# Performance work log

Hardware: AMD Instinct MI355X
Metric: run time of the kernel (lower is better)

The kernel has to match this reference:

```python
import jax, jax.numpy as jnp
import numpy as np

B, T, C = 8, 1024, 768
H = 12
HS = C // H  # 64


def setup_inputs() -> dict:
    key = jax.random.key(0)
    ks = jax.random.split(key, 6)
    s = C ** -0.5
    x = jax.random.normal(ks[0], (B, T, C), dtype=jnp.float32)
    Wq = jax.random.normal(ks[1], (H, C, HS), dtype=jnp.float32) * s
    Wk = jax.random.normal(ks[2], (H, C, HS), dtype=jnp.float32) * s
    Wv = jax.random.normal(ks[3], (H, C, HS), dtype=jnp.float32) * s
    Wproj = jax.random.normal(ks[4], (C, C), dtype=jnp.float32) * s
    bproj = jax.random.normal(ks[5], (C,), dtype=jnp.float32) * 0.01
    return {"x": x, "Wq": Wq, "Wk": Wk, "Wv": Wv, "Wproj": Wproj, "bproj": bproj}


def reference(x, Wq, Wk, Wv, Wproj, bproj):
    # per-head projections (equivalent to stacked per-head nn.Linear, bias=False)
    q = jnp.einsum('btc,hcd->bhtd', x, Wq)
    k = jnp.einsum('btc,hcd->bhtd', x, Wk)
    v = jnp.einsum('btc,hcd->bhtd', x, Wv)
    scale = HS ** -0.5
    scores = jnp.einsum('bhtd,bhsd->bhts', q, k) * scale  # [B,H,T,T]
    causal = jnp.tril(jnp.ones((T, T), dtype=bool))
    scores = jnp.where(causal, scores, -jnp.inf)
    weights = jax.nn.softmax(scores, axis=-1)
    out = jnp.einsum('bhts,bhsd->bhtd', weights, v)  # [B,H,T,HS]
    out = out.transpose(0, 2, 1, 3).reshape(B, T, C)  # concat heads
    # output projection (dropout is identity in eval mode)
    return out @ Wproj.T + bproj
```

## Files before the change

### kernel.cpp

```cpp
#include <hip/hip_runtime.h>
#include <hip/hip_bf16.h>


typedef short bf16x8 __attribute__((ext_vector_type(8)));
typedef short bf16x4 __attribute__((ext_vector_type(4)));
typedef float f32x4 __attribute__((ext_vector_type(4)));

static __device__ __forceinline__ unsigned short f2bf(float f) {
  unsigned int u = __float_as_uint(f);
  u += 0x7fffu + ((u >> 16) & 1u);
  return (unsigned short)(u >> 16);
}

static __device__ __forceinline__ unsigned int pk2bf(float a, float b) {
  union { __hip_bfloat162 h; unsigned int u; } c;
  c.h = __float22bfloat162_rn(make_float2(a, b));
  return c.u;
}

static __device__ __forceinline__ void gl_lds16(const void* g, void* l) {
  __builtin_amdgcn_global_load_lds(
      (const __attribute__((address_space(1))) unsigned int*)g,
      (__attribute__((address_space(3))) unsigned int*)l, 16, 0, 0);
}

__global__ __launch_bounds__(256) void k_prep(
    const float* __restrict__ x, const float* __restrict__ Wproj,
    const float* __restrict__ Wq, const float* __restrict__ Wk,
    const float* __restrict__ Wv,
    unsigned short* __restrict__ xb, unsigned short* __restrict__ wp,
    unsigned short* __restrict__ wt) {
  __shared__ float tb[64][65];
  const int bx = blockIdx.x;
  const int tid = threadIdx.x;
  if (bx < 6720) {
    const float* src = (bx < 6144) ? x : Wproj;
    unsigned short* dst = (bx < 6144) ? xb : wp;
    int i = (bx < 6144 ? bx : bx - 6144) * 256 + tid;
    float4 f = ((const float4*)src)[i];
    uint2 o;
    o.x = pk2bf(f.x, f.y);
    o.y = pk2bf(f.z, f.w);
    ((uint2*)dst)[i] = o;
    return;
  }
  const int idx = bx - 6720;
  const int c0 = (idx % 12) * 64;
  const int hq = idx / 12;
  const int qi = hq / 12, h = hq % 12;
  const float* W = (qi == 0) ? Wq : ((qi == 1) ? Wk : Wv);
  {
    int rowb = tid >> 4;
    int col4 = (tid & 15) * 4;
#pragma unroll
    for (int it = 0; it < 4; ++it) {
      int c = it * 16 + rowb;
      float4 f = *(const float4*)(W + (h * 768 + c0 + c) * 64 + col4);
      tb[c][col4] = f.x; tb[c][col4 + 1] = f.y; tb[c][col4 + 2] = f.z; tb[c][col4 + 3] = f.w;
    }
  }
  __syncthreads();
#pragma unroll
  for (int it = 0; it < 2; ++it) {
    int slot = it * 256 + tid;
    int d = slot >> 3, cg = (slot & 7) * 8;
    union { unsigned int u[4]; uint4 v; } o;
#pragma unroll
    for (int j = 0; j < 4; ++j)
      o.u[j] = pk2bf(tb[cg + 2 * j][d], tb[cg + 2 * j + 1][d]);
    *(uint4*)(wt + (qi * 768 + h * 64 + d) * 768 + c0 + cg) = o.v;
  }
}

__global__ __launch_bounds__(256) void k_gemm_qk(
    const unsigned short* __restrict__ xb,
    const unsigned short* __restrict__ wt,
    unsigned short* __restrict__ qkv) {
  __shared__ unsigned short As[128 * 32];
  __shared__ unsigned short Bs[128 * 32];
  const int tid = threadIdx.x;
  const int w = tid >> 6, lane = tid & 63, quad = lane >> 4, lr = lane & 15;
  const int wm = w >> 1, wn = w & 1;
  const int m0 = blockIdx.x * 128, n0 = blockIdx.y * 128;

  f32x4 acc[4][4] = {};

  const int srow = w * 16 + (lane >> 2);
  const int scol = (lane & 3) * 8;
  const unsigned short* ga0 = xb + (m0 + srow) * 768 + scol;
  const unsigned short* ga1 = ga0 + 64 * 768;
  const unsigned short* gb0 = wt + (n0 + srow) * 768 + scol;
  const unsigned short* gb1 = gb0 + 64 * 768;
  unsigned short* la0 = &As[(w * 16) * 32];
  unsigned short* la1 = la0 + 64 * 32;
  unsigned short* lb0 = &Bs[(w * 16) * 32];
  unsigned short* lb1 = lb0 + 64 * 32;

  for (int k0 = 0; k0 < 768; k0 += 32) {
    gl_lds16(ga0 + k0, la0);
    gl_lds16(ga1 + k0, la1);
    gl_lds16(gb0 + k0, lb0);
    gl_lds16(gb1 + k0, lb1);
    __syncthreads();
    bf16x8 af[4], bfr[4];
#pragma unroll
    for (int i = 0; i < 4; ++i)
      af[i] = *(const bf16x8*)(&As[(wm * 64 + i * 16 + lr) * 32 + quad * 8]);
#pragma unroll
    for (int j = 0; j < 4; ++j)
      bfr[j] = *(const bf16x8*)(&Bs[(wn * 64 + j * 16 + lr) * 32 + quad * 8]);
#pragma unroll
    for (int j = 0; j < 4; ++j)
#pragma unroll
      for (int i = 0; i < 4; ++i)
        acc[j][i] = __builtin_amdgcn_mfma_f32_16x16x32_bf16(bfr[j], af[i], acc[j][i], 0, 0, 0);
    __syncthreads();
  }

  const int b = m0 >> 10, t0 = m0 & 1023;
  const int qi = n0 / 768;
  const int rr0 = n0 - qi * 768;
#pragma unroll
  for (int j = 0; j < 4; ++j) {
    int nn = rr0 + wn * 64 + j * 16 + quad * 4;
    int h = nn >> 6, d0 = nn & 63;
    unsigned short* hb = qkv + (size_t)((qi * 8 + b) * 12 + h) * 65536 + d0;
#pragma unroll
    for (int i = 0; i < 4; ++i) {
      int t = t0 + wm * 64 + i * 16 + lr;
      uint2 o;
      o.x = pk2bf(acc[j][i][0], acc[j][i][1]);
      o.y = pk2bf(acc[j][i][2], acc[j][i][3]);
      *(uint2*)(hb + (size_t)t * 64) = o;
    }
  }
}

__global__ __launch_bounds__(256) void k_gemm_v(
    const unsigned short* __restrict__ xb,
    const unsigned short* __restrict__ wt,
    unsigned short* __restrict__ vt) {
  __shared__ unsigned short As[128 * 32];
  __shared__ unsigned short Bs[128 * 32];
  const int tid = threadIdx.x;
  const int w = tid >> 6, lane = tid & 63, quad = lane >> 4, lr = lane & 15;
  const int wm = w >> 1, wn = w & 1;
  const int m0 = blockIdx.x * 128, n0 = blockIdx.y * 128;

  f32x4 acc[4][4] = {};

  const int srow = w * 16 + (lane >> 2);
  const int scol = (lane & 3) * 8;
  const unsigned short* ga0 = xb + (m0 + srow) * 768 + scol;
  const unsigned short* ga1 = ga0 + 64 * 768;
  const unsigned short* gb0 = wt + (size_t)(1536 + n0 + srow) * 768 + scol;
  const unsigned short* gb1 = gb0 + 64 * 768;
  unsigned short* la0 = &As[(w * 16) * 32];
  unsigned short* la1 = la0 + 64 * 32;
  unsigned short* lb0 = &Bs[(w * 16) * 32];
  unsigned short* lb1 = lb0 + 64 * 32;

  for (int k0 = 0; k0 < 768; k0 += 32) {
    gl_lds16(ga0 + k0, la0);
    gl_lds16(ga1 + k0, la1);
    gl_lds16(gb0 + k0, lb0);
    gl_lds16(gb1 + k0, lb1);
    __syncthreads();
    bf16x8 af[4], bfr[4];
#pragma unroll
    for (int i = 0; i < 4; ++i)
      af[i] = *(const bf16x8*)(&As[(wm * 64 + i * 16 + lr) * 32 + quad * 8]);
#pragma unroll
    for (int j = 0; j < 4; ++j)
      bfr[j] = *(const bf16x8*)(&Bs[(wn * 64 + j * 16 + lr) * 32 + quad * 8]);
#pragma unroll
    for (int i = 0; i < 4; ++i)
#pragma unroll
      for (int j = 0; j < 4; ++j)
        acc[i][j] = __builtin_amdgcn_mfma_f32_16x16x32_bf16(af[i], bfr[j], acc[i][j], 0, 0, 0);
    __syncthreads();
  }

  const int b = m0 >> 10, t0 = m0 & 1023;
#pragma unroll
  for (int j = 0; j < 4; ++j) {
    int rr = n0 + wn * 64 + j * 16 + lr;
    int h = rr >> 6, d = rr & 63;
    unsigned short* vrow = vt + (size_t)((b * 12 + h) * 64 + d) * 1024;
#pragma unroll
    for (int i = 0; i < 4; ++i) {
      int t = t0 + wm * 64 + i * 16 + quad * 4;
      uint2 o;
      o.x = pk2bf(acc[i][j][0], acc[i][j][1]);
      o.y = pk2bf(acc[i][j][2], acc[i][j][3]);
      *(uint2*)(vrow + t) = o;
    }
  }
}

__global__ __launch_bounds__(256, 4) void k_attn(
    const unsigned short* __restrict__ qkv,
    const unsigned short* __restrict__ Vtg,
    unsigned short* __restrict__ attn) {
  __shared__ unsigned short Kbuf[2][64 * 64];
  __shared__ unsigned short Vbuf[2][64 * 64];
  const int tid = threadIdx.x;
  const int w = tid >> 6, lane = tid & 63, quad = lane >> 4, lr = lane & 15;
  const int hb = blockIdx.x;
  const int qb = 7 - (int)blockIdx.y;
  const int h = hb % 12, b = hb / 12;
  const int HT = 65536;
  const unsigned short* Q  = qkv + (b * 12 + h) * HT;
  const unsigned short* K  = qkv + (96 + b * 12 + h) * HT;
  const unsigned short* Vt = Vtg + (b * 12 + h) * HT;

  bf16x8 bq[2][2];
#pragma unroll
  for (int i = 0; i < 2; ++i)
#pragma unroll
    for (int hf = 0; hf < 2; ++hf)
      bq[i][hf] = *(const bf16x8*)(Q + (qb * 128 + w * 32 + i * 16 + lr) * 64 + hf * 32 + quad * 8);

  f32x4 accO[2][4] = {};
  f32x4 accL[2] = {};

  const int nc = 2 * qb + 2;
  const float c1 = 0.125f * 1.4426950408889634f;
  const float c0 = -4.0f * 1.4426950408889634f;
  const short one_bf = (short)0x3f80;
  const bf16x4 ones4 = {one_bf, one_bf, one_bf, one_bf};

  auto stage = [&](int bi, int sc) {
#pragma unroll
    for (int j = 0; j < 2; ++j) {
      int row = w * 16 + j * 8 + (lane >> 3);
      int c8 = (lane & 7) ^ (row & 7);
      gl_lds16(K + (sc * 64 + row) * 64 + c8 * 8, &Kbuf[bi][(w * 16 + j * 8) * 64]);
      gl_lds16(Vt + row * 1024 + sc * 64 + c8 * 8, &Vbuf[bi][(w * 16 + j * 8) * 64]);
    }
  };

  stage(0, 0);
  for (int sc = 0; sc < nc; ++sc) {
    __syncthreads();
    if (sc + 1 < nc) stage((sc + 1) & 1, sc + 1);
    const unsigned short* Kl = Kbuf[sc & 1];
    const unsigned short* Vl = Vbuf[sc & 1];

    f32x4 accT[2][4];
#pragma unroll
    for (int i = 0; i < 2; ++i)
#pragma unroll
      for (int nt = 0; nt < 4; ++nt) {
        f32x4 z = {};
#pragma unroll
        for (int hf = 0; hf < 2; ++hf) {
          int s = nt * 16 + lr;
          bf16x8 kb = *(const bf16x8*)(Kl + (s * 8 + ((4 * hf + quad) ^ (s & 7))) * 8);
          z = __builtin_amdgcn_mfma_f32_16x16x32_bf16(kb, bq[i][hf], z, 0, 0, 0);
        }
        accT[i][nt] = z;
      }

    bf16x4 pb[2][4];
#pragma unroll
    for (int i = 0; i < 2; ++i) {
      const int base_i = qb * 128 + w * 32 + i * 16;
      const bool needmask = (sc * 64 + 63 > base_i);
      const int q_l = base_i + lr;
#pragma unroll
      for (int st = 0; st < 4; ++st) {
        float p[4];
#pragma unroll
        for (int r = 0; r < 4; ++r) {
          float e = __builtin_amdgcn_exp2f(fmaf(accT[i][st][r], c1, c0));
          if (needmask && (sc * 64 + st * 16 + quad * 4 + r > q_l)) e = 0.f;
          p[r] = e;
        }
        union { unsigned int u[2]; bf16x4 v; } pk;
        pk.u[0] = pk2bf(p[0], p[1]);
        pk.u[1] = pk2bf(p[2], p[3]);
        pb[i][st] = pk.v;
        accL[i] = __builtin_amdgcn_mfma_f32_16x16x16bf16_1k(ones4, pb[i][st], accL[i], 0, 0, 0);
      }
    }

#pragma unroll
    for (int ntd = 0; ntd < 4; ++ntd) {
#pragma unroll
      for (int st = 0; st < 4; ++st) {
        int d = ntd * 16 + lr;
        int u = st * 2 + (quad >> 1);
        int us = u ^ (d & 7);
        bf16x4 va = *(const bf16x4*)(Vl + d * 64 + us * 8 + (quad & 1) * 4);
#pragma unroll
        for (int i = 0; i < 2; ++i)
          accO[i][ntd] = __builtin_amdgcn_mfma_f32_16x16x16bf16_1k(va, pb[i][st], accO[i][ntd], 0, 0, 0);
      }
    }
  }

  float linv[2];
#pragma unroll
  for (int i = 0; i < 2; ++i) linv[i] = 1.0f / accL[i][0];

#pragma unroll
  for (int i = 0; i < 2; ++i) {
    int t = qb * 128 + w * 32 + i * 16 + lr;
    unsigned short* row = attn + (size_t)(b * 1024 + t) * 768 + h * 64 + quad * 4;
#pragma unroll
    for (int ntd = 0; ntd < 4; ++ntd) {
      uint2 o;
      o.x = pk2bf(accO[i][ntd][0] * linv[i], accO[i][ntd][1] * linv[i]);
      o.y = pk2bf(accO[i][ntd][2] * linv[i], accO[i][ntd][3] * linv[i]);
      *(uint2*)(row + ntd * 16) = o;
    }
  }
}

__global__ __launch_bounds__(256) void k_gemm_proj(
    const unsigned short* __restrict__ ab,
    const unsigned short* __restrict__ wp,
    const float* __restrict__ bias,
    float* __restrict__ out) {
  __shared__ unsigned short As[128 * 32];
  __shared__ unsigned short Bs[128 * 32];
  const int tid = threadIdx.x;
  const int w = tid >> 6, lane = tid & 63, quad = lane >> 4, lr = lane & 15;
  const int wm = w >> 1, wn = w & 1;
  const int m0 = blockIdx.x * 128, n0 = blockIdx.y * 128;

  f32x4 acc[4][4] = {};

  const int srow = w * 16 + (lane >> 2);
  const int scol = (lane & 3) * 8;
  const unsigned short* ga0 = ab + (m0 + srow) * 768 + scol;
  const unsigned short* ga1 = ga0 + 64 * 768;
  const unsigned short* gb0 = wp + (n0 + srow) * 768 + scol;
  const unsigned short* gb1 = gb0 + 64 * 768;
  unsigned short* la0 = &As[(w * 16) * 32];
  unsigned short* la1 = la0 + 64 * 32;
  unsigned short* lb0 = &Bs[(w * 16) * 32];
  unsigned short* lb1 = lb0 + 64 * 32;

  for (int k0 = 0; k0 < 768; k0 += 32) {
    gl_lds16(ga0 + k0, la0);
    gl_lds16(ga1 + k0, la1);
    gl_lds16(gb0 + k0, lb0);
    gl_lds16(gb1 + k0, lb1);
    __syncthreads();
    bf16x8 af[4], bfr[4];
#pragma unroll
    for (int i = 0; i < 4; ++i)
      af[i] = *(const bf16x8*)(&As[(wm * 64 + i * 16 + lr) * 32 + quad * 8]);
#pragma unroll
    for (int j = 0; j < 4; ++j)
      bfr[j] = *(const bf16x8*)(&Bs[(wn * 64 + j * 16 + lr) * 32 + quad * 8]);
#pragma unroll
    for (int j = 0; j < 4; ++j)
#pragma unroll
      for (int i = 0; i < 4; ++i)
        acc[j][i] = __builtin_amdgcn_mfma_f32_16x16x32_bf16(bfr[j], af[i], acc[j][i], 0, 0, 0);
    __syncthreads();
  }

#pragma unroll
  for (int j = 0; j < 4; ++j) {
    int ncol = n0 + wn * 64 + j * 16 + quad * 4;
    float4 bv = *(const float4*)(bias + ncol);
#pragma unroll
    for (int i = 0; i < 4; ++i) {
      int m = m0 + wm * 64 + i * 16 + lr;
      float4 v;
      v.x = acc[j][i][0] + bv.x;
      v.y = acc[j][i][1] + bv.y;
      v.z = acc[j][i][2] + bv.z;
      v.w = acc[j][i][3] + bv.w;
      *(float4*)(out + (size_t)m * 768 + ncol) = v;
    }
  }
}

extern "C" void kernel_launch(void* const* d_in, const int* in_sizes, int n_in,
                              void* d_out, int out_size, void* d_ws, size_t ws_size,
                              hipStream_t stream) {
  const float* x     = (const float*)d_in[0];
  const float* Wq    = (const float*)d_in[1];
  const float* Wk    = (const float*)d_in[2];
  const float* Wv    = (const float*)d_in[3];
  const float* Wproj = (const float*)d_in[4];
  const float* bproj = (const float*)d_in[5];
  float* out = (float*)d_out;

  char* p = (char*)d_ws;
  unsigned short* xb   = (unsigned short*)p; p += 12582912;
  unsigned short* wt   = (unsigned short*)p; p += 3538944;
  unsigned short* wp   = (unsigned short*)p; p += 1179648;
  unsigned short* qkv  = (unsigned short*)p; p += 37748736;
  unsigned short* attn = (unsigned short*)p; p += 12582912;
  unsigned short* vt   = qkv + (size_t)192 * 65536;

  k_prep<<<7152, 256, 0, stream>>>(x, Wproj, Wq, Wk, Wv, xb, wp, wt);
  k_gemm_qk<<<dim3(64, 12), 256, 0, stream>>>(xb, wt, qkv);
  k_gemm_v<<<dim3(64, 6), 256, 0, stream>>>(xb, wt, vt);
  k_attn<<<dim3(96, 8), 256, 0, stream>>>(qkv, vt, attn);
  k_gemm_proj<<<dim3(64, 6), 256, 0, stream>>>(attn, wp, bproj, out);
}
```

Before: 200.7 us.

## Route attention probabilities through LDS and use 16x16x32 MFMA for PV

The attention kernel now computes scores as S = Q·K^T rather than K·Q^T. It writes the exponentiated probabilities into a per-wave LDS buffer and reads them back as 8-wide A operands, so the P·V product uses the 16x16x32 bf16 MFMA instead of the 16x16x16 one. The row sums are kept in registers and reduced with lane shuffles, which replaces the ones-vector MFMA. The cost is extra LDS traffic and shared memory per block, the occupancy hint in launch_bounds is dropped, and the output stores become scalar 2-byte writes instead of packed 8-byte ones.

New measurement: 195.0 us. 1.03x faster.

```diff
diff --git a/kernel.cpp b/kernel.cpp
--- a/kernel.cpp
+++ b/kernel.cpp
@@ -3,7 +3,6 @@
 
 
 typedef short bf16x8 __attribute__((ext_vector_type(8)));
-typedef short bf16x4 __attribute__((ext_vector_type(4)));
 typedef float f32x4 __attribute__((ext_vector_type(4)));
 
 static __device__ __forceinline__ unsigned short f2bf(float f) {
@@ -198,12 +197,13 @@
   }
 }
 
-__global__ __launch_bounds__(256, 4) void k_attn(
+__global__ __launch_bounds__(256) void k_attn(
     const unsigned short* __restrict__ qkv,
     const unsigned short* __restrict__ Vtg,
     unsigned short* __restrict__ attn) {
   __shared__ unsigned short Kbuf[2][64 * 64];
   __shared__ unsigned short Vbuf[2][64 * 64];
+  __shared__ unsigned short Pbuf[4][32 * 68];
   const int tid = threadIdx.x;
   const int w = tid >> 6, lane = tid & 63, quad = lane >> 4, lr = lane & 15;
   const int hb = blockIdx.x;
@@ -214,21 +214,19 @@
   const unsigned short* K  = qkv + (96 + b * 12 + h) * HT;
   const unsigned short* Vt = Vtg + (b * 12 + h) * HT;
 
-  bf16x8 bq[2][2];
+  bf16x8 aq[2][2];
 #pragma unroll
   for (int i = 0; i < 2; ++i)
 #pragma unroll
     for (int hf = 0; hf < 2; ++hf)
-      bq[i][hf] = *(const bf16x8*)(Q + (qb * 128 + w * 32 + i * 16 + lr) * 64 + hf * 32 + quad * 8);
+      aq[i][hf] = *(const bf16x8*)(Q + (qb * 128 + w * 32 + i * 16 + lr) * 64 + hf * 32 + quad * 8);
 
   f32x4 accO[2][4] = {};
-  f32x4 accL[2] = {};
+  float lsum[2][4] = {};
 
   const int nc = 2 * qb + 2;
   const float c1 = 0.125f * 1.4426950408889634f;
   const float c0 = -4.0f * 1.4426950408889634f;
-  const short one_bf = (short)0x3f80;
-  const bf16x4 ones4 = {one_bf, one_bf, one_bf, one_bf};
 
   auto stage = [&](int bi, int sc) {
 #pragma unroll
@@ -247,7 +245,7 @@
     const unsigned short* Kl = Kbuf[sc & 1];
     const unsigned short* Vl = Vbuf[sc & 1];
 
-    f32x4 accT[2][4];
+    f32x4 accS[2][4];
 #pragma unroll
     for (int i = 0; i < 2; ++i)
 #pragma unroll
@@ -257,65 +255,78 @@
         for (int hf = 0; hf < 2; ++hf) {
           int s = nt * 16 + lr;
           bf16x8 kb = *(const bf16x8*)(Kl + (s * 8 + ((4 * hf + quad) ^ (s & 7))) * 8);
-          z = __builtin_amdgcn_mfma_f32_16x16x32_bf16(kb, bq[i][hf], z, 0, 0, 0);
+          z = __builtin_amdgcn_mfma_f32_16x16x32_bf16(aq[i][hf], kb, z, 0, 0, 0);
         }
-        accT[i][nt] = z;
+        accS[i][nt] = z;
       }
 
-    bf16x4 pb[2][4];
 #pragma unroll
     for (int i = 0; i < 2; ++i) {
       const int base_i = qb * 128 + w * 32 + i * 16;
       const bool needmask = (sc * 64 + 63 > base_i);
-      const int q_l = base_i + lr;
-#pragma unroll
-      for (int st = 0; st < 4; ++st) {
+#pragma unroll
+      for (int r = 0; r < 4; ++r) {
+        int tg = base_i + quad * 4 + r;
+        unsigned short* prow = &Pbuf[w][(i * 16 + quad * 4 + r) * 68 + lr];
         float p[4];
 #pragma unroll
-        for (int r = 0; r < 4; ++r) {
-          float e = __builtin_amdgcn_exp2f(fmaf(accT[i][st][r], c1, c0));
-          if (needmask && (sc * 64 + st * 16 + quad * 4 + r > q_l)) e = 0.f;
-          p[r] = e;
+        for (int nt = 0; nt < 4; ++nt) {
+          float e = __builtin_amdgcn_exp2f(fmaf(accS[i][nt][r], c1, c0));
+          if (needmask && (sc * 64 + nt * 16 + lr > tg)) e = 0.f;
+          lsum[i][r] += e;
+          p[nt] = e;
         }
-        union { unsigned int u[2]; bf16x4 v; } pk;
-        pk.u[0] = pk2bf(p[0], p[1]);
-        pk.u[1] = pk2bf(p[2], p[3]);
-        pb[i][st] = pk.v;
-        accL[i] = __builtin_amdgcn_mfma_f32_16x16x16bf16_1k(ones4, pb[i][st], accL[i], 0, 0, 0);
+        unsigned int u01 = pk2bf(p[0], p[1]);
+        unsigned int u23 = pk2bf(p[2], p[3]);
+        prow[0]  = (unsigned short)(u01 & 0xffffu);
+        prow[16] = (unsigned short)(u01 >> 16);
+        prow[32] = (unsigned short)(u23 & 0xffffu);
+        prow[48] = (unsigned short)(u23 >> 16);
       }
     }
 
 #pragma unroll
+    for (int i = 0; i < 2; ++i) {
+      bf16x8 pa[2];
+#pragma unroll
+      for (int hf = 0; hf < 2; ++hf)
+        pa[hf] = *(const bf16x8*)(&Pbuf[w][(i * 16 + lr) * 68 + hf * 32 + quad * 8]);
+#pragma unroll
+      for (int ntd = 0; ntd < 4; ++ntd) {
+        int d = ntd * 16 + lr;
+#pragma unroll
+        for (int hf = 0; hf < 2; ++hf) {
+          bf16x8 vb = *(const bf16x8*)(Vl + (d * 8 + ((4 * hf + quad) ^ (d & 7))) * 8);
+          accO[i][ntd] = __builtin_amdgcn_mfma_f32_16x16x32_bf16(pa[hf], vb, accO[i][ntd], 0, 0, 0);
+        }
+      }
+    }
+  }
+
+  float linv[2][4];
+#pragma unroll
+  for (int i = 0; i < 2; ++i)
+#pragma unroll
+    for (int r = 0; r < 4; ++r) {
+      float l = lsum[i][r];
+      l += __shfl_xor(l, 1);
+      l += __shfl_xor(l, 2);
+      l += __shfl_xor(l, 4);
+      l += __shfl_xor(l, 8);
+      linv[i][r] = 1.0f / l;
+    }
+
+#pragma unroll
+  for (int i = 0; i < 2; ++i)
+#pragma unroll
     for (int ntd = 0; ntd < 4; ++ntd) {
-#pragma unroll
-      for (int st = 0; st < 4; ++st) {
-        int d = ntd * 16 + lr;
-        int u = st * 2 + (quad >> 1);
-        int us = u ^ (d & 7);
-        bf16x4 va = *(const bf16x4*)(Vl + d * 64 + us * 8 + (quad & 1) * 4);
-#pragma unroll
-        for (int i = 0; i < 2; ++i)
-          accO[i][ntd] = __builtin_amdgcn_mfma_f32_16x16x16bf16_1k(va, pb[i][st], accO[i][ntd], 0, 0, 0);
+      int c = h * 64 + ntd * 16 + lr;
+#pragma unroll
+      for (int r = 0; r < 4; ++r) {
+        int t = qb * 128 + w * 32 + i * 16 + quad * 4 + r;
+        attn[(b * 1024 + t) * 768 + c] = f2bf(accO[i][ntd][r] * linv[i][r]);
       }
     }
-  }
-
-  float linv[2];
-#pragma unroll
-  for (int i = 0; i < 2; ++i) linv[i] = 1.0f / accL[i][0];
-
-#pragma unroll
-  for (int i = 0; i < 2; ++i) {
-    int t = qb * 128 + w * 32 + i * 16 + lr;
-    unsigned short* row = attn + (size_t)(b * 1024 + t) * 768 + h * 64 + quad * 4;
-#pragma unroll
-    for (int ntd = 0; ntd < 4; ++ntd) {
-      uint2 o;
-      o.x = pk2bf(accO[i][ntd][0] * linv[i], accO[i][ntd][1] * linv[i]);
-      o.y = pk2bf(accO[i][ntd][2] * linv[i], accO[i][ntd][3] * linv[i]);
-      *(uint2*)(row + ntd * 16) = o;
-    }
-  }
 }
 
 __global__ __launch_bounds__(256) void k_gemm_proj(
```
